# Performance work log

Measured on AMD Instinct MI355X. Metric: run time of the kernel, lower is better.

The kernel has to match this reference:

```python
import jax, jax.numpy as jnp
import numpy as np

SL, BS, HS, FFN, E, TOPK = 2048, 4, 1024, 4096, 8, 2
T = SL * BS

def setup_inputs() -> dict:
    key = jax.random.key(0)
    k1, k2, k3, k4, k5, k6 = jax.random.split(key, 6)
    x = jax.random.normal(k1, (SL, BS, HS), dtype=jnp.float32)
    expert_weights = jax.random.uniform(k2, (T, TOPK), dtype=jnp.float32)
    expert_indices = jax.random.randint(k3, (T, TOPK), 0, E).astype(jnp.int64)
    scores = jax.random.uniform(k4, (T, TOPK), dtype=jnp.float32)
    w1 = jax.random.normal(k5, (E, HS, FFN), dtype=jnp.float32) * 0.02
    w2 = jax.random.normal(k6, (E, FFN, HS), dtype=jnp.float32) * 0.02
    return {"x": x, "expert_weights": expert_weights, "scores": scores,
            "w1": w1, "w2": w2, "expert_indices": expert_indices}

def reference(x, expert_weights, scores, w1, w2, expert_indices):
    # Dropless MoE dispatch-compute-combine with router_type=None.
    # Math identity: megablocks gather/grouped-GEMM/scatter with per-copy
    # expert_weights equals, for each token t:
    #   out[t] = sum_k expert_weights[t,k] * MLP_{e(t,k)}(x[t])
    # We fold the top-k copies into a per-(token, expert) combine weight and
    # run one GEMM pair per expert (fixed small E), matching the grouped GEMM.
    sl, bs, hs = x.shape
    num_experts = w1.shape[0]
    xf = x.reshape(-1, hs)  # [T, hs]
    onehot = jax.nn.one_hot(expert_indices, num_experts, dtype=x.dtype)  # [T, k, E]
    combine = jnp.einsum("tk,tke->et", expert_weights, onehot)  # [E, T]

    def expert_step(acc, inputs):
        w1e, w2e, cw = inputs  # [hs, ffn], [ffn, hs], [T]
        h = jax.nn.gelu(xf @ w1e, approximate=False)  # [T, ffn]
        acc = acc + cw[:, None] * (h @ w2e)  # [T, hs]
        return acc, None

    out, _ = jax.lax.scan(expert_step, jnp.zeros_like(xf), (w1, w2, combine))
    return out.reshape(sl, bs, hs)
```

## Files before the change

kernel.cpp:

```cpp
#include <hip/hip_runtime.h>
#include <hip/hip_bf16.h>
#include <math.h>
#include <stdint.h>

#define N_TOK   8192
#define HS      1024
#define FFN     4096
#define NE      8
#define NA      16384
#define CAP     16384
#define BM      256
#define MAXT    72

typedef __attribute__((ext_vector_type(8))) short          bf16x8;
typedef __attribute__((ext_vector_type(4))) float          f32x4;
typedef __attribute__((ext_vector_type(4))) float          fvec4;
typedef __attribute__((ext_vector_type(4))) unsigned short usvec4;

__device__ __forceinline__ void gl_lds16(const void* g, void* l) {
  __builtin_amdgcn_global_load_lds(
      (const __attribute__((address_space(1))) unsigned int*)g,
      (__attribute__((address_space(3))) unsigned int*)l,
      16, 0, 0);
}

__device__ __forceinline__ unsigned short f2bf(float f) {
  union { float f; unsigned int u; } v; v.f = f;
  unsigned int r = v.u + 0x7FFFu + ((v.u >> 16) & 1u);
  return (unsigned short)(r >> 16);
}


__global__ void cvt_x_kernel(const fvec4* __restrict__ in, unsigned short* __restrict__ out, int n4) {
  int i = blockIdx.x * 256 + threadIdx.x;
  if (i >= n4) return;
  fvec4 v = in[i];
  usvec4 o;
  o[0] = f2bf(v[0]); o[1] = f2bf(v[1]); o[2] = f2bf(v[2]); o[3] = f2bf(v[3]);
  *(usvec4*)(out + (size_t)i * 4) = o;
}

__global__ void tpose_cvt_kernel(const float* __restrict__ in, unsigned short* __restrict__ out,
                                 int R, int C) {
  __shared__ float t[64][65];
  int bc = blockIdx.x * 64, br = blockIdx.y * 64, e = blockIdx.z;
  const float* ine = in + (size_t)e * R * C;
  unsigned short* oute = out + (size_t)e * R * C;
  int tx = threadIdx.x & 63, ty = threadIdx.x >> 6;
#pragma unroll
  for (int q = 0; q < 16; ++q) {
    int r = ty * 16 + q;
    t[r][tx] = ine[(size_t)(br + r) * C + bc + tx];
  }
  __syncthreads();
#pragma unroll
  for (int q = 0; q < 16; ++q) {
    int c = ty * 16 + q;
    oute[(size_t)(bc + c) * R + br + tx] = f2bf(t[tx][c]);
  }
}


__global__ void route_kernel(const int* __restrict__ idx, const float* __restrict__ wts,
                             int* __restrict__ counts, int* __restrict__ btok,
                             int* __restrict__ bslot, float* __restrict__ bw) {
  int a = blockIdx.x * 256 + threadIdx.x;
  if (a >= NA) return;
  int e = idx[a];
  int pos = atomicAdd(&counts[e], 1);
  btok[(size_t)e * CAP + pos]  = a >> 1;
  bslot[(size_t)e * CAP + pos] = a;
  bw[(size_t)e * CAP + pos]    = wts[a];
}

__global__ void build_tiles_kernel(int* __restrict__ counts, int2* __restrict__ table) {
  if (threadIdx.x == 0 && blockIdx.x == 0) {
    int nt = 0;
    for (int e = 0; e < NE; ++e) {
      int c = counts[e];
      int t = (c + BM - 1) >> 8;
      for (int m = 0; m < t && nt < MAXT; ++m) table[nt++] = make_int2(e, m);
    }
    counts[8] = nt;
  }
}

template <int EPI, int KDIM>
__global__ __launch_bounds__(512, 2)
void moe_gemm(const unsigned short* __restrict__ Ab,
              const unsigned short* __restrict__ Bb,
              unsigned short* __restrict__ hout,
              float* __restrict__ perm,
              const int* __restrict__ btok,
              const int* __restrict__ bslot,
              const float* __restrict__ bw,
              const int* __restrict__ counts,
              const int2* __restrict__ table,
              int p0, int tc) {
  constexpr int NCOLS = (EPI == 0) ? (FFN / 256) : (HS / 256);
  constexpr int NSLAB = KDIM / 64;
  constexpr int SLABSZ = 65536;

  __shared__ char lds[2 * SLABSZ];

  int bid = blockIdx.x;
  int j = bid / NCOLS;
  int bn0 = (bid % NCOLS) * 256;

  int nt = counts[8];
  if (j < p0 || j >= p0 + tc || j >= nt) return;
  int2 te = table[j];
  int e = te.x, tm = te.y;
  int count = counts[e];
  int slotb = j - p0;

  int tid = threadIdx.x;
  int wid = tid >> 6, lane = tid & 63;
  int wm = wid >> 2, wn = wid & 3;

  const unsigned short* Be = Bb + (size_t)e * ((size_t)FFN * HS);

  const char* src[8];
  int dst[8];
  int lrow8 = lane >> 3;
  int klog = ((lane & 7) * 16) ^ (lrow8 << 4);
#pragma unroll
  for (int q = 0; q < 8; ++q) {
    int c = wid * 8 + q;
    dst[q] = c * 1024;
    if (c < 32) {
      int row = c * 8 + lrow8;
      if (EPI == 0) {
        int grow = tm * BM + row;
        int tok = (grow < count) ? btok[(size_t)e * CAP + grow] : 0;
        src[q] = (const char*)(Ab + (size_t)tok * KDIM) + klog;
      } else {
        src[q] = (const char*)(Ab + ((size_t)slotb * BM + row) * KDIM) + klog;
      }
    } else {
      int nrow = bn0 + (c - 32) * 8 + lrow8;
      src[q] = (const char*)(Be + (size_t)nrow * KDIM) + klog;
    }
  }

  int rA = wm * 128 + (lane & 15);
  int rB = wn * 64 + (lane & 15);
  int ksw = (lane >> 4) * 16;
  int swz = (lane & 7) << 4;
  int offA[2], offB[2];
#pragma unroll
  for (int kk = 0; kk < 2; ++kk) {
    offA[kk] = rA * 128 + ((kk * 64 + ksw) ^ swz);
    offB[kk] = 32768 + rB * 128 + ((kk * 64 + ksw) ^ swz);
  }

  f32x4 acc[8][4] = {};

#pragma unroll
  for (int q = 0; q < 8; ++q) gl_lds16(src[q], lds + dst[q]);
  asm volatile("s_waitcnt vmcnt(0)" ::: "memory");
  __builtin_amdgcn_s_barrier();
  __builtin_amdgcn_sched_barrier(0);

  for (int t = 0; t < NSLAB; ++t) {
    char* rbuf = lds + (t & 1) * SLABSZ;
    char* db   = lds + ((t + 1) & 1) * SLABSZ;
    if (t + 1 < NSLAB) {
#pragma unroll
      for (int q = 0; q < 8; ++q)
        gl_lds16(src[q] + (size_t)(t + 1) * 128, db + dst[q]);
    }
#pragma unroll
    for (int kk = 0; kk < 2; ++kk) {
      bf16x8 a[8], b[4];
#pragma unroll
      for (int n = 0; n < 4; ++n) b[n] = *(const bf16x8*)(rbuf + offB[kk] + n * 2048);
#pragma unroll
      for (int i = 0; i < 8; ++i) a[i] = *(const bf16x8*)(rbuf + offA[kk] + i * 2048);
#pragma unroll
      for (int i = 0; i < 8; ++i)
#pragma unroll
        for (int n = 0; n < 4; ++n)
          acc[i][n] = __builtin_amdgcn_mfma_f32_16x16x32_bf16(a[i], b[n], acc[i][n], 0, 0, 0);
    }
    __builtin_amdgcn_sched_barrier(0);
    asm volatile("s_waitcnt vmcnt(0)" ::: "memory");
    __builtin_amdgcn_s_barrier();
    __builtin_amdgcn_sched_barrier(0);
  }

  char* wlds = lds + wid * 8192;
  int l15 = lane & 15, l16 = lane >> 4;
#pragma unroll
  for (int p = 0; p < 4; ++p) {
#pragma unroll
    for (int ii = 0; ii < 2; ++ii) {
      int i = p * 2 + ii;
#pragma unroll
      for (int n = 0; n < 4; ++n) {
        int waddr = (ii * 16 + l16 * 4) * 256 + (n * 16 + l15) * 4;
#pragma unroll
        for (int rr = 0; rr < 4; ++rr)
          *(float*)(wlds + waddr + rr * 256) = acc[i][n][rr];
      }
    }
    asm volatile("s_waitcnt lgkmcnt(0)" ::: "memory");
    __builtin_amdgcn_sched_barrier(0);
#pragma unroll
    for (int rd = 0; rd < 8; ++rd) {
      int row = rd * 4 + l16;
      f32x4 v = *(const f32x4*)(wlds + row * 256 + l15 * 16);
      int col = bn0 + wn * 64 + l15 * 4;
      if (EPI == 0) {
        usvec4 o;
#pragma unroll
        for (int z = 0; z < 4; ++z) {
          float vv = v[z];
          float x2 = vv * vv;
          float u2 = 1.5957691216057308f * vv * fmaf(0.044715f, x2, 1.0f);
          u2 = fminf(fmaxf(u2, -30.f), 30.f);
          float ee = __expf(u2);
          o[z] = f2bf(vv * __fdividef(ee, ee + 1.0f));
        }
        size_t hrow = (size_t)slotb * BM + wm * 128 + p * 32 + row;
        *(usvec4*)(hout + hrow * FFN + col) = o;
      } else {
        int grow = tm * BM + wm * 128 + p * 32 + row;
        if (grow < count) {
          int s = bslot[(size_t)e * CAP + grow];
          float wgt = bw[(size_t)e * CAP + grow];
          fvec4 o;
#pragma unroll
          for (int z = 0; z < 4; ++z) o[z] = wgt * v[z];
          *(fvec4*)(perm + (size_t)s * HS + col) = o;
        }
      }
    }
    __builtin_amdgcn_sched_barrier(0);
  }
}

__global__ void combine_kernel(const fvec4* __restrict__ perm, fvec4* __restrict__ out, int n4) {
  int i = blockIdx.x * 256 + threadIdx.x;
  if (i >= n4) return;
  int t = i >> 8;
  int c = i & 255;
  out[i] = perm[(size_t)(2 * t) * 256 + c] + perm[(size_t)(2 * t + 1) * 256 + c];
}


extern "C" void kernel_launch(void* const* d_in, const int* in_sizes, int n_in,
                              void* d_out, int out_size, void* d_ws, size_t ws_size,
                              hipStream_t stream) {
  const float* x   = (const float*)d_in[0];
  const float* ew  = (const float*)d_in[1];
  const float* w1  = (const float*)d_in[3];
  const float* w2  = (const float*)d_in[4];
  const int*   eix = (const int*)d_in[5];

  char* ws = (char*)d_ws;
  const size_t o_w1T    = 0;
  const size_t o_w2T    = 67108864ULL;
  const size_t o_xb     = 134217728ULL;
  const size_t o_btok   = 150994944ULL;
  const size_t o_bslot  = 151519232ULL;
  const size_t o_bw     = 152043520ULL;
  const size_t o_counts = 152567808ULL;
  const size_t o_table  = 152568064ULL;
  const size_t o_perm   = 152569344ULL;
  const size_t o_h      = 219678208ULL;

  unsigned short* w1T = (unsigned short*)(ws + o_w1T);
  unsigned short* w2T = (unsigned short*)(ws + o_w2T);
  unsigned short* xb  = (unsigned short*)(ws + o_xb);
  int*   btok   = (int*)(ws + o_btok);
  int*   bslot  = (int*)(ws + o_bslot);
  float* bw     = (float*)(ws + o_bw);
  int*   counts = (int*)(ws + o_counts);
  int2*  table  = (int2*)(ws + o_table);
  float* perm   = (float*)(ws + o_perm);
  unsigned short* hbuf = (unsigned short*)(ws + o_h);

  long long havail = (long long)ws_size - (long long)o_h;
  long long tile_bytes = (long long)BM * FFN * 2;
  int tc = (int)(havail / tile_bytes);
  if (tc < 1) tc = 1;
  if (tc > MAXT) tc = MAXT;
  int npass = (MAXT + tc - 1) / tc;

  hipMemsetAsync(counts, 0, 256, stream);

  cvt_x_kernel<<<(N_TOK * HS / 4 + 255) / 256, 256, 0, stream>>>(
      (const fvec4*)x, xb, N_TOK * HS / 4);
  tpose_cvt_kernel<<<dim3(FFN / 64, HS / 64, NE), 256, 0, stream>>>(w1, w1T, HS, FFN);
  tpose_cvt_kernel<<<dim3(HS / 64, FFN / 64, NE), 256, 0, stream>>>(w2, w2T, FFN, HS);

  route_kernel<<<(NA + 255) / 256, 256, 0, stream>>>(eix, ew, counts, btok, bslot, bw);
  build_tiles_kernel<<<1, 64, 0, stream>>>(counts, table);

  for (int p = 0; p < npass; ++p) {
    moe_gemm<0, HS><<<dim3(MAXT * 16), 512, 0, stream>>>(
        xb, w1T, hbuf, perm, btok, bslot, bw, counts, table, p * tc, tc);
    moe_gemm<1, FFN><<<dim3(MAXT * 4), 512, 0, stream>>>(
        hbuf, w2T, hbuf, perm, btok, bslot, bw, counts, table, p * tc, tc);
  }

  combine_kernel<<<(N_TOK * HS / 4 + 255) / 256, 256, 0, stream>>>(
      (const fvec4*)perm, (fvec4*)d_out, N_TOK * HS / 4);
}
```

Before: 615.3 us.

## Use 128x128 tiles with persistent atomic work queue and split-K second GEMM

Shrinks the GEMM tile from 256x256 with 512 threads to 128x128 with 256 threads and a K-step of 32. The grid becomes persistent: blocks pull work units from an atomic counter, so the ragged per-expert tile set packs onto the CUs with less tail imbalance. The second GEMM is split into two K halves that write separate perm buffers, which the combine kernel then sums. The smaller tiles lower arithmetic intensity and add extra perm traffic and workspace, but should give better load balance and occupancy.

```diff
diff --git a/kernel.cpp b/kernel.cpp
--- a/kernel.cpp
+++ b/kernel.cpp
@@ -9,8 +9,9 @@
 #define NE      8
 #define NA      16384
 #define CAP     16384
-#define BM      256
-#define MAXT    72
+#define BMT     128
+#define MAXT    136
+#define PERMSZ  16777216ULL
 
 typedef __attribute__((ext_vector_type(8))) short          bf16x8;
 typedef __attribute__((ext_vector_type(4))) float          f32x4;
@@ -78,15 +79,15 @@
     int nt = 0;
     for (int e = 0; e < NE; ++e) {
       int c = counts[e];
-      int t = (c + BM - 1) >> 8;
+      int t = (c + BMT - 1) >> 7;
       for (int m = 0; m < t && nt < MAXT; ++m) table[nt++] = make_int2(e, m);
     }
     counts[8] = nt;
   }
 }
 
-template <int EPI, int KDIM>
-__global__ __launch_bounds__(512, 2)
+template <int EPI, int AROW, int KTOT, int NU>
+__global__ __launch_bounds__(256, 3)
 void moe_gemm(const unsigned short* __restrict__ Ab,
               const unsigned short* __restrict__ Bb,
               unsigned short* __restrict__ hout,
@@ -96,147 +97,149 @@
               const float* __restrict__ bw,
               const int* __restrict__ counts,
               const int2* __restrict__ table,
-              int p0, int tc) {
-  constexpr int NCOLS = (EPI == 0) ? (FFN / 256) : (HS / 256);
-  constexpr int NSLAB = KDIM / 64;
-  constexpr int SLABSZ = 65536;
-
-  __shared__ char lds[2 * SLABSZ];
-
-  int bid = blockIdx.x;
-  int j = bid / NCOLS;
-  int bn0 = (bid % NCOLS) * 256;
-
-  int nt = counts[8];
-  if (j < p0 || j >= p0 + tc || j >= nt) return;
-  int2 te = table[j];
-  int e = te.x, tm = te.y;
-  int count = counts[e];
-  int slotb = j - p0;
+              int* __restrict__ ctr, int p0, int tc) {
+  constexpr int NT = KTOT / 32;
+  __shared__ char lds[32768];
+  __shared__ int s_u;
 
   int tid = threadIdx.x;
   int wid = tid >> 6, lane = tid & 63;
-  int wm = wid >> 2, wn = wid & 3;
-
-  const unsigned short* Be = Bb + (size_t)e * ((size_t)FFN * HS);
-
-  const char* src[8];
-  int dst[8];
-  int lrow8 = lane >> 3;
-  int klog = ((lane & 7) * 16) ^ (lrow8 << 4);
-#pragma unroll
-  for (int q = 0; q < 8; ++q) {
-    int c = wid * 8 + q;
-    dst[q] = c * 1024;
-    if (c < 32) {
-      int row = c * 8 + lrow8;
-      if (EPI == 0) {
-        int grow = tm * BM + row;
-        int tok = (grow < count) ? btok[(size_t)e * CAP + grow] : 0;
-        src[q] = (const char*)(Ab + (size_t)tok * KDIM) + klog;
+  int wm = wid >> 1, wn = wid & 1;
+  int nt = counts[8];
+
+  int rin = lane >> 2;
+  int klog = ((lane & 3) * 16) ^ (((rin >> 1) & 3) << 4);
+  int dst[4];
+#pragma unroll
+  for (int q = 0; q < 4; ++q) dst[q] = (wid * 4 + q) * 1024;
+
+  int l15 = lane & 15, l16 = lane >> 4;
+  int swzr = ((l15 >> 1) & 3) << 4;
+  int ks = l16 * 16;
+  int offA0 = (wm * 64 + l15) * 64 + (ks ^ swzr);
+  int offB0 = 8192 + (wn * 64 + l15) * 64 + (ks ^ swzr);
+
+  for (;;) {
+    __syncthreads();
+    if (tid == 0) s_u = atomicAdd(ctr, 1);
+    __syncthreads();
+    int u = s_u;
+    if (u >= NU) return;
+
+    int kq, col, j;
+    if (EPI == 0) { kq = 0; col = u / MAXT; j = u % MAXT; }
+    else          { kq = u / (8 * MAXT); int rem = u % (8 * MAXT); col = rem / MAXT; j = rem % MAXT; }
+    if (j >= nt || j < p0 || j >= p0 + tc) continue;
+    int2 te = table[j];
+    int e = te.x, tm = te.y;
+    int count = counts[e];
+    int slotb = j - p0;
+    int bn0 = col * 128;
+    int kbyte0 = kq * (KTOT * 2);
+
+    const unsigned short* Be = Bb + (size_t)e * ((size_t)FFN * HS);
+
+    const char* src[4];
+#pragma unroll
+    for (int q = 0; q < 4; ++q) {
+      int c = wid * 4 + q;
+      if (c < 8) {
+        int row = c * 16 + rin;
+        if (EPI == 0) {
+          int grow = tm * BMT + row;
+          int tok = (grow < count) ? btok[(size_t)e * CAP + grow] : 0;
+          src[q] = (const char*)(Ab + (size_t)tok * AROW) + kbyte0 + klog;
+        } else {
+          src[q] = (const char*)(Ab + ((size_t)slotb * BMT + row) * AROW) + kbyte0 + klog;
+        }
       } else {
-        src[q] = (const char*)(Ab + ((size_t)slotb * BM + row) * KDIM) + klog;
+        int nrow = bn0 + (c - 8) * 16 + rin;
+        src[q] = (const char*)(Be + (size_t)nrow * AROW) + kbyte0 + klog;
       }
-    } else {
-      int nrow = bn0 + (c - 32) * 8 + lrow8;
-      src[q] = (const char*)(Be + (size_t)nrow * KDIM) + klog;
     }
-  }
-
-  int rA = wm * 128 + (lane & 15);
-  int rB = wn * 64 + (lane & 15);
-  int ksw = (lane >> 4) * 16;
-  int swz = (lane & 7) << 4;
-  int offA[2], offB[2];
-#pragma unroll
-  for (int kk = 0; kk < 2; ++kk) {
-    offA[kk] = rA * 128 + ((kk * 64 + ksw) ^ swz);
-    offB[kk] = 32768 + rB * 128 + ((kk * 64 + ksw) ^ swz);
-  }
-
-  f32x4 acc[8][4] = {};
-
-#pragma unroll
-  for (int q = 0; q < 8; ++q) gl_lds16(src[q], lds + dst[q]);
-  asm volatile("s_waitcnt vmcnt(0)" ::: "memory");
-  __builtin_amdgcn_s_barrier();
-  __builtin_amdgcn_sched_barrier(0);
-
-  for (int t = 0; t < NSLAB; ++t) {
-    char* rbuf = lds + (t & 1) * SLABSZ;
-    char* db   = lds + ((t + 1) & 1) * SLABSZ;
-    if (t + 1 < NSLAB) {
-#pragma unroll
-      for (int q = 0; q < 8; ++q)
-        gl_lds16(src[q] + (size_t)(t + 1) * 128, db + dst[q]);
-    }
-#pragma unroll
-    for (int kk = 0; kk < 2; ++kk) {
-      bf16x8 a[8], b[4];
-#pragma unroll
-      for (int n = 0; n < 4; ++n) b[n] = *(const bf16x8*)(rbuf + offB[kk] + n * 2048);
-#pragma unroll
-      for (int i = 0; i < 8; ++i) a[i] = *(const bf16x8*)(rbuf + offA[kk] + i * 2048);
-#pragma unroll
-      for (int i = 0; i < 8; ++i)
-#pragma unroll
-        for (int n = 0; n < 4; ++n)
-          acc[i][n] = __builtin_amdgcn_mfma_f32_16x16x32_bf16(a[i], b[n], acc[i][n], 0, 0, 0);
-    }
-    __builtin_amdgcn_sched_barrier(0);
+
+    f32x4 acc[4][4] = {};
+
+#pragma unroll
+    for (int q = 0; q < 4; ++q) gl_lds16(src[q], lds + dst[q]);
     asm volatile("s_waitcnt vmcnt(0)" ::: "memory");
     __builtin_amdgcn_s_barrier();
     __builtin_amdgcn_sched_barrier(0);
-  }
-
-  char* wlds = lds + wid * 8192;
-  int l15 = lane & 15, l16 = lane >> 4;
-#pragma unroll
-  for (int p = 0; p < 4; ++p) {
-#pragma unroll
-    for (int ii = 0; ii < 2; ++ii) {
-      int i = p * 2 + ii;
-#pragma unroll
-      for (int n = 0; n < 4; ++n) {
-        int waddr = (ii * 16 + l16 * 4) * 256 + (n * 16 + l15) * 4;
-#pragma unroll
-        for (int rr = 0; rr < 4; ++rr)
-          *(float*)(wlds + waddr + rr * 256) = acc[i][n][rr];
+
+    for (int t = 0; t < NT; ++t) {
+      const char* rbuf = lds + (t & 1) * 16384;
+      char* db = lds + ((t + 1) & 1) * 16384;
+      if (t + 1 < NT) {
+#pragma unroll
+        for (int q = 0; q < 4; ++q)
+          gl_lds16(src[q] + (size_t)(t + 1) * 64, db + dst[q]);
       }
+      bf16x8 a[4], b[4];
+#pragma unroll
+      for (int n = 0; n < 4; ++n) b[n] = *(const bf16x8*)(rbuf + offB0 + n * 1024);
+#pragma unroll
+      for (int i = 0; i < 4; ++i) a[i] = *(const bf16x8*)(rbuf + offA0 + i * 1024);
+      __builtin_amdgcn_s_setprio(1);
+#pragma unroll
+      for (int i = 0; i < 4; ++i)
+#pragma unroll
+        for (int n = 0; n < 4; ++n)
+          acc[i][n] = __builtin_amdgcn_mfma_f32_16x16x32_bf16(a[i], b[n], acc[i][n], 0, 0, 0);
+      __builtin_amdgcn_s_setprio(0);
+      __builtin_amdgcn_sched_barrier(0);
+      asm volatile("s_waitcnt vmcnt(0)" ::: "memory");
+      __builtin_amdgcn_s_barrier();
+      __builtin_amdgcn_sched_barrier(0);
     }
-    asm volatile("s_waitcnt lgkmcnt(0)" ::: "memory");
-    __builtin_amdgcn_sched_barrier(0);
-#pragma unroll
-    for (int rd = 0; rd < 8; ++rd) {
-      int row = rd * 4 + l16;
-      f32x4 v = *(const f32x4*)(wlds + row * 256 + l15 * 16);
-      int col = bn0 + wn * 64 + l15 * 4;
-      if (EPI == 0) {
-        usvec4 o;
-#pragma unroll
-        for (int z = 0; z < 4; ++z) {
-          float vv = v[z];
-          float x2 = vv * vv;
-          float u2 = 1.5957691216057308f * vv * fmaf(0.044715f, x2, 1.0f);
-          u2 = fminf(fmaxf(u2, -30.f), 30.f);
-          float ee = __expf(u2);
-          o[z] = f2bf(vv * __fdividef(ee, ee + 1.0f));
-        }
-        size_t hrow = (size_t)slotb * BM + wm * 128 + p * 32 + row;
-        *(usvec4*)(hout + hrow * FFN + col) = o;
-      } else {
-        int grow = tm * BM + wm * 128 + p * 32 + row;
-        if (grow < count) {
-          int s = bslot[(size_t)e * CAP + grow];
-          float wgt = bw[(size_t)e * CAP + grow];
-          fvec4 o;
-#pragma unroll
-          for (int z = 0; z < 4; ++z) o[z] = wgt * v[z];
-          *(fvec4*)(perm + (size_t)s * HS + col) = o;
+
+    char* wlds = lds + wid * 8192;
+#pragma unroll
+    for (int p = 0; p < 2; ++p) {
+#pragma unroll
+      for (int ii = 0; ii < 2; ++ii) {
+        int i = p * 2 + ii;
+#pragma unroll
+        for (int n = 0; n < 4; ++n) {
+          int waddr = (ii * 16 + l16 * 4) * 256 + (n * 16 + l15) * 4;
+#pragma unroll
+          for (int rr = 0; rr < 4; ++rr)
+            *(float*)(wlds + waddr + rr * 256) = acc[i][n][rr];
         }
       }
+      asm volatile("s_waitcnt lgkmcnt(0)" ::: "memory");
+      __builtin_amdgcn_sched_barrier(0);
+#pragma unroll
+      for (int rd = 0; rd < 8; ++rd) {
+        int row = rd * 4 + l16;
+        f32x4 v = *(const f32x4*)(wlds + row * 256 + l15 * 16);
+        int colg = bn0 + wn * 64 + l15 * 4;
+        if (EPI == 0) {
+          usvec4 o;
+#pragma unroll
+          for (int z = 0; z < 4; ++z) {
+            float vv = v[z];
+            float x2 = vv * vv;
+            float u2 = 1.5957691216057308f * vv * fmaf(0.044715f, x2, 1.0f);
+            u2 = fminf(fmaxf(u2, -30.f), 30.f);
+            float ee = __expf(u2);
+            o[z] = f2bf(vv * __fdividef(ee, ee + 1.0f));
+          }
+          size_t hrow = (size_t)slotb * BMT + wm * 64 + p * 32 + row;
+          *(usvec4*)(hout + hrow * FFN + colg) = o;
+        } else {
+          int grow = tm * BMT + wm * 64 + p * 32 + row;
+          if (grow < count) {
+            int s = bslot[(size_t)e * CAP + grow];
+            float wgt = bw[(size_t)e * CAP + grow];
+            fvec4 o;
+#pragma unroll
+            for (int z = 0; z < 4; ++z) o[z] = wgt * v[z];
+            *(fvec4*)(perm + (size_t)kq * PERMSZ + (size_t)s * HS + colg) = o;
+          }
+        }
+      }
+      __builtin_amdgcn_sched_barrier(0);
     }
-    __builtin_amdgcn_sched_barrier(0);
   }
 }
 
@@ -245,7 +248,11 @@
   if (i >= n4) return;
   int t = i >> 8;
   int c = i & 255;
-  out[i] = perm[(size_t)(2 * t) * 256 + c] + perm[(size_t)(2 * t + 1) * 256 + c];
+  const fvec4* p0 = perm;
+  const fvec4* p1 = perm + PERMSZ / 4;
+  size_t r0 = (size_t)(2 * t) * 256 + c;
+  size_t r1 = (size_t)(2 * t + 1) * 256 + c;
+  out[i] = (p0[r0] + p1[r0]) + (p0[r1] + p1[r1]);
 }
 
 
@@ -267,8 +274,9 @@
   const size_t o_bw     = 152043520ULL;
   const size_t o_counts = 152567808ULL;
   const size_t o_table  = 152568064ULL;
-  const size_t o_perm   = 152569344ULL;
-  const size_t o_h      = 219678208ULL;
+  const size_t o_ctr    = 152570112ULL;
+  const size_t o_perm   = 152572160ULL;
+  const size_t o_h      = 286789888ULL;
 
   unsigned short* w1T = (unsigned short*)(ws + o_w1T);
   unsigned short* w2T = (unsigned short*)(ws + o_w2T);
@@ -278,17 +286,20 @@
   float* bw     = (float*)(ws + o_bw);
   int*   counts = (int*)(ws + o_counts);
   int2*  table  = (int2*)(ws + o_table);
+  int*   ctrs   = (int*)(ws + o_ctr);
   float* perm   = (float*)(ws + o_perm);
   unsigned short* hbuf = (unsigned short*)(ws + o_h);
 
   long long havail = (long long)ws_size - (long long)o_h;
-  long long tile_bytes = (long long)BM * FFN * 2;
+  long long tile_bytes = (long long)BMT * FFN * 2;
   int tc = (int)(havail / tile_bytes);
   if (tc < 1) tc = 1;
   if (tc > MAXT) tc = MAXT;
   int npass = (MAXT + tc - 1) / tc;
+  if (npass > 128) npass = 128;
 
   hipMemsetAsync(counts, 0, 256, stream);
+  hipMemsetAsync(ctrs, 0, 2048, stream);
 
   cvt_x_kernel<<<(N_TOK * HS / 4 + 255) / 256, 256, 0, stream>>>(
       (const fvec4*)x, xb, N_TOK * HS / 4);
@@ -299,10 +310,12 @@
   build_tiles_kernel<<<1, 64, 0, stream>>>(counts, table);
 
   for (int p = 0; p < npass; ++p) {
-    moe_gemm<0, HS><<<dim3(MAXT * 16), 512, 0, stream>>>(
-        xb, w1T, hbuf, perm, btok, bslot, bw, counts, table, p * tc, tc);
-    moe_gemm<1, FFN><<<dim3(MAXT * 4), 512, 0, stream>>>(
-        hbuf, w2T, hbuf, perm, btok, bslot, bw, counts, table, p * tc, tc);
+    moe_gemm<0, HS, HS, 32 * MAXT><<<dim3(1024), 256, 0, stream>>>(
+        xb, w1T, hbuf, perm, btok, bslot, bw, counts, table,
+        &ctrs[p * 2 + 0], p * tc, tc);
+    moe_gemm<1, FFN, FFN / 2, 2 * 8 * MAXT><<<dim3(1024), 256, 0, stream>>>(
+        hbuf, w2T, hbuf, perm, btok, bslot, bw, counts, table,
+        &ctrs[p * 2 + 1], p * tc, tc);
   }
 
   combine_kernel<<<(N_TOK * HS / 4 + 255) / 256, 256, 0, stream>>>(
```

Result: slower. 684.1 us (+11.2%).
